# Kernel optimization log

Hardware: AMD Instinct MI355X
Metric: run time of the kernel (lower is better)

## Reference

```python
import jax, jax.numpy as jnp
import numpy as np

B, T, C, H = 4, 2048, 1024, 16
HD = C // H  # head_dim = 64


def setup_inputs() -> dict:
    key = jax.random.key(0)
    ks = jax.random.split(key, 6)
    s_in = 1.0 / np.sqrt(C)
    x = jax.random.normal(ks[0], (B, T, C), dtype=jnp.float32)
    # per-head projection weights, stacked over heads: [H, C, HD]
    Wq = jax.random.uniform(ks[1], (H, C, HD), dtype=jnp.float32, minval=-s_in, maxval=s_in)
    Wk = jax.random.uniform(ks[2], (H, C, HD), dtype=jnp.float32, minval=-s_in, maxval=s_in)
    Wv = jax.random.uniform(ks[3], (H, C, HD), dtype=jnp.float32, minval=-s_in, maxval=s_in)
    # output projection (torch Linear: weight [out,in], bias [out])
    Wp = jax.random.uniform(ks[4], (C, C), dtype=jnp.float32, minval=-s_in, maxval=s_in)
    bp = jax.random.uniform(ks[5], (C,), dtype=jnp.float32, minval=-s_in, maxval=s_in)
    return {"x": x, "Wq": Wq, "Wk": Wk, "Wv": Wv, "Wp": Wp, "bp": bp}


def reference(x, Wq, Wk, Wv, Wp, bp):
    Bx, Tx, Cx = x.shape
    scale = Cx ** 0.5  # NOTE: original scales by embed_dim**0.5, not head_dim**0.5
    q = jnp.einsum('btc,hcd->bhtd', x, Wq)
    k = jnp.einsum('btc,hcd->bhtd', x, Wk)
    v = jnp.einsum('btc,hcd->bhtd', x, Wv)
    # original: einsum('btc,bTc->bTt', q, k) -> logits[b, i, j] = q[b, j] . k[b, i]
    logits = jnp.einsum('bhjd,bhid->bhij', q, k) / scale
    causal = jnp.tril(jnp.ones((Tx, Tx), dtype=bool))  # mask j > i
    logits = jnp.where(causal[None, None], logits, jnp.float32(-jnp.inf))
    weights = jax.nn.softmax(logits, axis=-1)  # [B,H,T,T], the returned attention maps
    # original: einsum('btt,btc->btc', weights, value) -> diagonal of weights scales value
    diag = jnp.diagonal(weights, axis1=-2, axis2=-1)  # [B,H,T]
    attn = diag[..., None] * v  # [B,H,T,HD]
    cat = attn.transpose(0, 2, 1, 3).reshape(Bx, Tx, Cx)  # concat heads on last dim
    out = cat @ Wp.T + bp  # dropout p=0.0 -> identity
    return out, weights
```

## Files before the change

kernel.cpp:

```cpp
#include <hip/hip_runtime.h>


#define NB 4
#define NT 2048
#define NC 1024
#define NH 16
#define NHD 64
#define BH (NB * NH)
typedef unsigned short ushort_t;
#define SLAB ((size_t)NT * (size_t)NT)

typedef __attribute__((ext_vector_type(8))) short short8;
typedef __attribute__((ext_vector_type(4))) float f32x4;

__device__ __forceinline__ ushort_t f2bf(float f) {
    unsigned int x = __float_as_uint(f);
    x += 0x7fffu + ((x >> 16) & 1u);
    return (ushort_t)(x >> 16);
}
__device__ __forceinline__ float bf2f(ushort_t u) {
    return __uint_as_float(((unsigned int)u) << 16);
}

#define GLD_LDS16(g, l) \
    __builtin_amdgcn_global_load_lds( \
        (const __attribute__((address_space(1))) unsigned int*)(g), \
        (__attribute__((address_space(3))) unsigned int*)(l), 16, 0, 0)

__global__ __launch_bounds__(256) void cvt_x(
    const float* __restrict__ x, ushort_t* __restrict__ xbf)
{
    const size_t o = ((size_t)blockIdx.x * 256 + threadIdx.x) * 4;
    float4 u = *(const float4*)(x + o);
    ushort4 v;
    v.x = f2bf(u.x); v.y = f2bf(u.y); v.z = f2bf(u.z); v.w = f2bf(u.w);
    *(ushort4*)(xbf + o) = v;
}

__global__ __launch_bounds__(256) void cvt_w(
    const float* __restrict__ Wq, const float* __restrict__ Wk,
    const float* __restrict__ Wv, ushort_t* __restrict__ Wt)
{
    const int o = blockIdx.x * 256 + threadIdx.x;
    const int sel = o >> 20;
    const int h = (o >> 16) & 15;
    const int idx = o & 65535;
    const int d = idx >> 10, c = idx & 1023;
    const float* W = (sel == 0 ? Wq : (sel == 1 ? Wk : Wv));
    Wt[o] = f2bf(W[(size_t)h * 65536 + (size_t)c * 64 + d]);
}

__global__ __launch_bounds__(256) void cvt_wp(
    const float* __restrict__ Wp, ushort_t* __restrict__ Wpb)
{
    const size_t o = ((size_t)blockIdx.x * 256 + threadIdx.x) * 4;
    float4 u = *(const float4*)(Wp + o);
    ushort4 v;
    v.x = f2bf(u.x); v.y = f2bf(u.y); v.z = f2bf(u.z); v.w = f2bf(u.w);
    *(ushort4*)(Wpb + o) = v;
}

__global__ __launch_bounds__(256) void qkv_gemm2(
    const ushort_t* __restrict__ xbf, const ushort_t* __restrict__ Wt,
    ushort_t* __restrict__ qo, ushort_t* __restrict__ ko, ushort_t* __restrict__ vo)
{
    __shared__ ushort_t smA[128 * 64];
    __shared__ ushort_t smB[128 * 64];
    const int n0 = blockIdx.x * 128;
    const int m0 = blockIdx.y * 128;
    const int tid = threadIdx.x;
    const int wid = tid >> 6, l = tid & 63, lr = l & 15, lg = l >> 4;
    const int wr = wid >> 1, wc = wid & 1;

    const int srow = wid * 32 + (l >> 3);
    const int scol0 = ((l & 7) ^ (srow & 7)) * 8;

    f32x4 acc[4][4];
    #pragma unroll
    for (int i = 0; i < 4; ++i)
        #pragma unroll
        for (int j = 0; j < 4; ++j) acc[i][j] = (f32x4){0.f, 0.f, 0.f, 0.f};

    for (int k0 = 0; k0 < NC; k0 += 64) {
        #pragma unroll
        for (int j = 0; j < 4; ++j) {
            const int row = srow + j * 8;
            GLD_LDS16(xbf + (size_t)(m0 + row) * NC + k0 + scol0,
                      &smA[wid * 2048 + j * 512]);
            GLD_LDS16(Wt + (size_t)(n0 + row) * NC + k0 + scol0,
                      &smB[wid * 2048 + j * 512]);
        }
        __syncthreads();
        short8 a[4][2], b[4][2];
        #pragma unroll
        for (int mi = 0; mi < 4; ++mi) {
            const int rowA = 64 * wr + 16 * mi + lr;
            const int sw = (rowA & 7) * 8;
            a[mi][0] = *(const short8*)&smA[rowA * 64 + ((8 * lg) ^ sw)];
            a[mi][1] = *(const short8*)&smA[rowA * 64 + ((32 + 8 * lg) ^ sw)];
        }
        #pragma unroll
        for (int ni = 0; ni < 4; ++ni) {
            const int rowB = 64 * wc + 16 * ni + lr;
            const int sw = (rowB & 7) * 8;
            b[ni][0] = *(const short8*)&smB[rowB * 64 + ((8 * lg) ^ sw)];
            b[ni][1] = *(const short8*)&smB[rowB * 64 + ((32 + 8 * lg) ^ sw)];
        }
        #pragma unroll
        for (int mi = 0; mi < 4; ++mi)
            #pragma unroll
            for (int ni = 0; ni < 4; ++ni) {
                acc[mi][ni] = __builtin_amdgcn_mfma_f32_16x16x32_bf16(
                    a[mi][0], b[ni][0], acc[mi][ni], 0, 0, 0);
                acc[mi][ni] = __builtin_amdgcn_mfma_f32_16x16x32_bf16(
                    a[mi][1], b[ni][1], acc[mi][ni], 0, 0, 0);
            }
        __syncthreads();
    }
    const int selh = blockIdx.x * 2 + wc;
    const int sel = selh >> 4, h = selh & 15;
    ushort_t* outp = (sel == 0 ? qo : (sel == 1 ? ko : vo));
    #pragma unroll
    for (int mi = 0; mi < 4; ++mi) {
        #pragma unroll
        for (int r = 0; r < 4; ++r) {
            const int m = m0 + 64 * wr + 16 * mi + 4 * lg + r;
            const int bb = m >> 11, tt = m & 2047;
            ushort_t* orow = outp + ((size_t)(bb * NH + h) * NT + tt) * NHD;
            #pragma unroll
            for (int ni = 0; ni < 4; ++ni)
                orow[16 * ni + lr] = f2bf(acc[mi][ni][r]);
        }
    }
}

__global__ __launch_bounds__(256) void scores_mfma(
    const ushort_t* __restrict__ q, const ushort_t* __restrict__ k,
    float* __restrict__ w, float* __restrict__ diag)
{
    __shared__ ushort_t smQ[64 * 64];
    const int ib = blockIdx.x, bh = blockIdx.y;
    const int tid = threadIdx.x;
    const int wid = tid >> 6, l = tid & 63, lr = l & 15, lg = l >> 4;
    const int i0 = ib * 64;
    const ushort_t* kb = k + (size_t)bh * (NT * NHD);
    const ushort_t* qb = q + (size_t)bh * (NT * NHD);
    float* wbase = w + (size_t)bh * SLAB;

    short8 af0, af1;
    {
        const ushort_t* kp = kb + (size_t)(i0 + wid * 16 + lr) * NHD + 8 * lg;
        af0 = *(const short8*)kp;
        af1 = *(const short8*)(kp + 32);
    }
    const int gi_base = i0 + wid * 16 + 4 * lg;

    const int srlo = l >> 3;
    const int scol = ((l & 7) ^ srlo) * 8;

    float lsum[4] = {0.f, 0.f, 0.f, 0.f};
    for (int jt = 0; jt <= ib; ++jt) {
        #pragma unroll
        for (int j = 0; j < 2; ++j) {
            const int row = wid * 16 + j * 8 + srlo;
            GLD_LDS16(qb + (size_t)(jt * 64 + row) * NHD + scol,
                      &smQ[(wid * 16 + j * 8) * 64]);
        }
        __syncthreads();
        #pragma unroll
        for (int nt = 0; nt < 4; ++nt) {
            const int rowB = nt * 16 + lr;
            const int sw = (rowB & 7) * 8;
            const short8 b0 = *(const short8*)&smQ[rowB * 64 + ((8 * lg) ^ sw)];
            const short8 b1 = *(const short8*)&smQ[rowB * 64 + ((32 + 8 * lg) ^ sw)];
            f32x4 acc = {0,0,0,0};
            acc = __builtin_amdgcn_mfma_f32_16x16x32_bf16(af0, b0, acc, 0, 0, 0);
            acc = __builtin_amdgcn_mfma_f32_16x16x32_bf16(af1, b1, acc, 0, 0, 0);
            const int gj = jt * 64 + nt * 16 + lr;
            #pragma unroll
            for (int r = 0; r < 4; ++r) {
                float e = __expf(acc[r] * 0.03125f);
                lsum[r] += (gj <= gi_base + r) ? e : 0.f;
            }
        }
        __syncthreads();
    }
    float linv[4];
    #pragma unroll
    for (int r = 0; r < 4; ++r) {
        float v = lsum[r];
        v += __shfl_xor(v, 1);
        v += __shfl_xor(v, 2);
        v += __shfl_xor(v, 4);
        v += __shfl_xor(v, 8);
        linv[r] = 1.0f / v;
    }
    for (int jt = 0; jt <= ib; ++jt) {
        #pragma unroll
        for (int j = 0; j < 2; ++j) {
            const int row = wid * 16 + j * 8 + srlo;
            GLD_LDS16(qb + (size_t)(jt * 64 + row) * NHD + scol,
                      &smQ[(wid * 16 + j * 8) * 64]);
        }
        __syncthreads();
        #pragma unroll
        for (int nt = 0; nt < 4; ++nt) {
            const int rowB = nt * 16 + lr;
            const int sw = (rowB & 7) * 8;
            const short8 b0 = *(const short8*)&smQ[rowB * 64 + ((8 * lg) ^ sw)];
            const short8 b1 = *(const short8*)&smQ[rowB * 64 + ((32 + 8 * lg) ^ sw)];
            f32x4 acc = {0,0,0,0};
            acc = __builtin_amdgcn_mfma_f32_16x16x32_bf16(af0, b0, acc, 0, 0, 0);
            acc = __builtin_amdgcn_mfma_f32_16x16x32_bf16(af1, b1, acc, 0, 0, 0);
            const int gj = jt * 64 + nt * 16 + lr;
            #pragma unroll
            for (int r = 0; r < 4; ++r) {
                const int gi = gi_base + r;
                float e = __expf(acc[r] * 0.03125f) * linv[r];
                e = (gj <= gi) ? e : 0.f;
                wbase[(size_t)gi * NT + gj] = e;
                if (gj == gi) diag[(size_t)bh * NT + gi] = e;
            }
        }
        __syncthreads();
    }
    for (int jt = ib + 1; jt < NT / 64; ++jt) {
        #pragma unroll
        for (int it = 0; it < 4; ++it) {
            const int row = i0 + wid * 16 + it * 4 + lg;
            *(float4*)&wbase[(size_t)row * NT + jt * 64 + lr * 4] =
                make_float4(0.f, 0.f, 0.f, 0.f);
        }
    }
}

__global__ __launch_bounds__(256) void scale_v(
    const ushort_t* __restrict__ v, const float* __restrict__ diag,
    ushort_t* __restrict__ vd)
{
    const size_t o8 = (size_t)blockIdx.x * 256 + threadIdx.x;
    const size_t o = o8 * 8;
    const size_t bht = o >> 6;
    const float dg = diag[bht];
    short8 u = *(const short8*)(v + o);
    short8 r;
    #pragma unroll
    for (int j = 0; j < 8; ++j)
        r[j] = (short)f2bf(bf2f((ushort_t)u[j]) * dg);
    *(short8*)(vd + o) = r;
}

__global__ __launch_bounds__(256) void out_gemm(
    const ushort_t* __restrict__ vd, const ushort_t* __restrict__ Wpb,
    const float* __restrict__ bpv, float* __restrict__ out)
{
    __shared__ ushort_t smA[128 * 64];
    __shared__ ushort_t smB[128 * 64];
    const int n0 = blockIdx.x * 128;
    const int m0 = blockIdx.y * 128;
    const int tid = threadIdx.x;
    const int wid = tid >> 6, l = tid & 63, lr = l & 15, lg = l >> 4;
    const int wr = wid >> 1, wc = wid & 1;

    const int srow = wid * 32 + (l >> 3);
    const int scol0 = ((l & 7) ^ (srow & 7)) * 8;

    f32x4 acc[4][4];
    #pragma unroll
    for (int i = 0; i < 4; ++i)
        #pragma unroll
        for (int j = 0; j < 4; ++j) acc[i][j] = (f32x4){0.f, 0.f, 0.f, 0.f};

    for (int k0 = 0; k0 < NC; k0 += 64) {
        const int h = k0 >> 6;
        #pragma unroll
        for (int j = 0; j < 4; ++j) {
            const int row = srow + j * 8;
            const int m = m0 + row, bb = m >> 11, tt = m & 2047;
            GLD_LDS16(vd + ((size_t)(bb * NH + h) * NT + tt) * NHD + scol0,
                      &smA[wid * 2048 + j * 512]);
            GLD_LDS16(Wpb + (size_t)(n0 + row) * NC + k0 + scol0,
                      &smB[wid * 2048 + j * 512]);
        }
        __syncthreads();
        short8 a[4][2], b[4][2];
        #pragma unroll
        for (int mi = 0; mi < 4; ++mi) {
            const int rowA = 64 * wr + 16 * mi + lr;
            const int sw = (rowA & 7) * 8;
            a[mi][0] = *(const short8*)&smA[rowA * 64 + ((8 * lg) ^ sw)];
            a[mi][1] = *(const short8*)&smA[rowA * 64 + ((32 + 8 * lg) ^ sw)];
        }
        #pragma unroll
        for (int ni = 0; ni < 4; ++ni) {
            const int rowB = 64 * wc + 16 * ni + lr;
            const int sw = (rowB & 7) * 8;
            b[ni][0] = *(const short8*)&smB[rowB * 64 + ((8 * lg) ^ sw)];
            b[ni][1] = *(const short8*)&smB[rowB * 64 + ((32 + 8 * lg) ^ sw)];
        }
        #pragma unroll
        for (int mi = 0; mi < 4; ++mi)
            #pragma unroll
            for (int ni = 0; ni < 4; ++ni) {
                acc[mi][ni] = __builtin_amdgcn_mfma_f32_16x16x32_bf16(
                    a[mi][0], b[ni][0], acc[mi][ni], 0, 0, 0);
                acc[mi][ni] = __builtin_amdgcn_mfma_f32_16x16x32_bf16(
                    a[mi][1], b[ni][1], acc[mi][ni], 0, 0, 0);
            }
        __syncthreads();
    }
    float bias[4];
    #pragma unroll
    for (int ni = 0; ni < 4; ++ni) bias[ni] = bpv[n0 + 64 * wc + 16 * ni + lr];
    #pragma unroll
    for (int mi = 0; mi < 4; ++mi) {
        #pragma unroll
        for (int r = 0; r < 4; ++r) {
            const int m = m0 + 64 * wr + 16 * mi + 4 * lg + r;
            float* orow = out + (size_t)m * NC + n0 + 64 * wc;
            #pragma unroll
            for (int ni = 0; ni < 4; ++ni)
                orow[16 * ni + lr] = acc[mi][ni][r] + bias[ni];
        }
    }
}

extern "C" void kernel_launch(void* const* d_in, const int* in_sizes, int n_in,
                              void* d_out, int out_size, void* d_ws, size_t ws_size,
                              hipStream_t stream)
{
    const float* x  = (const float*)d_in[0];
    const float* Wq = (const float*)d_in[1];
    const float* Wk = (const float*)d_in[2];
    const float* Wv = (const float*)d_in[3];
    const float* Wp = (const float*)d_in[4];
    const float* bp = (const float*)d_in[5];

    float* out = (float*)d_out;
    float* w = out + (size_t)NB * NT * NC;

    ushort_t* xbf = (ushort_t*)d_ws;
    ushort_t* Wt  = xbf + (size_t)NB * NT * NC;
    ushort_t* qs  = Wt + (size_t)3 * NH * NHD * NC;
    ushort_t* ks  = qs + (size_t)BH * NT * NHD;
    ushort_t* vs  = ks + (size_t)BH * NT * NHD;
    float* diag   = (float*)(vs + (size_t)BH * NT * NHD);
    ushort_t* Wpb = (ushort_t*)(diag + (size_t)BH * NT);
    ushort_t* vd  = Wpb + (size_t)NC * NC;

    cvt_x<<<(NB * NT * NC) / 1024, 256, 0, stream>>>(x, xbf);
    cvt_w<<<(3 * NH * NHD * NC) / 256, 256, 0, stream>>>(Wq, Wk, Wv, Wt);
    cvt_wp<<<(NC * NC) / 1024, 256, 0, stream>>>(Wp, Wpb);
    qkv_gemm2<<<dim3(24, 64), 256, 0, stream>>>(xbf, Wt, qs, ks, vs);
    scores_mfma<<<dim3(NT / 64, BH), 256, 0, stream>>>(qs, ks, w, diag);
    scale_v<<<(BH * NT * NHD) / (256 * 8), 256, 0, stream>>>(vs, diag, vd);
    out_gemm<<<dim3(8, 64), 256, 0, stream>>>(vd, Wpb, bp, out);
}
```

Measured before the change: 451.3 us.

## Fuse diag scaling into output GEMM, double-buffer Q tiles, use nontemporal stores

Removes the separate scale_v kernel by applying the softmax diagonal scale to V while staging it into shared memory in the output GEMM. The scores kernel now double-buffers Q tiles in LDS, prefetching the next tile during compute. The attention-weight, zero-fill and output writes become nontemporal stores to reduce cache pollution on the large streaming write. In exchange, the V loads in the GEMM go through registers instead of direct-to-LDS loads, and the kernel uses more LDS.

```diff
diff --git a/kernel.cpp b/kernel.cpp
--- a/kernel.cpp
+++ b/kernel.cpp
@@ -138,7 +138,7 @@
     const ushort_t* __restrict__ q, const ushort_t* __restrict__ k,
     float* __restrict__ w, float* __restrict__ diag)
 {
-    __shared__ ushort_t smQ[64 * 64];
+    __shared__ ushort_t smQ[2][64 * 64];
     const int ib = blockIdx.x, bh = blockIdx.y;
     const int tid = threadIdx.x;
     const int wid = tid >> 6, l = tid & 63, lr = l & 15, lg = l >> 4;
@@ -158,21 +158,26 @@
     const int srlo = l >> 3;
     const int scol = ((l & 7) ^ srlo) * 8;
 
+    #define STAGEQ(buf, jt)                                                  \
+        _Pragma("unroll")                                                    \
+        for (int j = 0; j < 2; ++j) {                                        \
+            const int row_ = wid * 16 + j * 8 + srlo;                        \
+            GLD_LDS16(qb + (size_t)((jt) * 64 + row_) * NHD + scol,          \
+                      &smQ[buf][(wid * 16 + j * 8) * 64]);                   \
+        }
+
     float lsum[4] = {0.f, 0.f, 0.f, 0.f};
+    STAGEQ(0, 0);
+    __syncthreads();
     for (int jt = 0; jt <= ib; ++jt) {
-        #pragma unroll
-        for (int j = 0; j < 2; ++j) {
-            const int row = wid * 16 + j * 8 + srlo;
-            GLD_LDS16(qb + (size_t)(jt * 64 + row) * NHD + scol,
-                      &smQ[(wid * 16 + j * 8) * 64]);
-        }
-        __syncthreads();
+        const int cur = jt & 1;
+        if (jt < ib) { STAGEQ(cur ^ 1, jt + 1); }
         #pragma unroll
         for (int nt = 0; nt < 4; ++nt) {
             const int rowB = nt * 16 + lr;
             const int sw = (rowB & 7) * 8;
-            const short8 b0 = *(const short8*)&smQ[rowB * 64 + ((8 * lg) ^ sw)];
-            const short8 b1 = *(const short8*)&smQ[rowB * 64 + ((32 + 8 * lg) ^ sw)];
+            const short8 b0 = *(const short8*)&smQ[cur][rowB * 64 + ((8 * lg) ^ sw)];
+            const short8 b1 = *(const short8*)&smQ[cur][rowB * 64 + ((32 + 8 * lg) ^ sw)];
             f32x4 acc = {0,0,0,0};
             acc = __builtin_amdgcn_mfma_f32_16x16x32_bf16(af0, b0, acc, 0, 0, 0);
             acc = __builtin_amdgcn_mfma_f32_16x16x32_bf16(af1, b1, acc, 0, 0, 0);
@@ -195,20 +200,17 @@
         v += __shfl_xor(v, 8);
         linv[r] = 1.0f / v;
     }
+    STAGEQ(0, 0);
+    __syncthreads();
     for (int jt = 0; jt <= ib; ++jt) {
-        #pragma unroll
-        for (int j = 0; j < 2; ++j) {
-            const int row = wid * 16 + j * 8 + srlo;
-            GLD_LDS16(qb + (size_t)(jt * 64 + row) * NHD + scol,
-                      &smQ[(wid * 16 + j * 8) * 64]);
-        }
-        __syncthreads();
+        const int cur = jt & 1;
+        if (jt < ib) { STAGEQ(cur ^ 1, jt + 1); }
         #pragma unroll
         for (int nt = 0; nt < 4; ++nt) {
             const int rowB = nt * 16 + lr;
             const int sw = (rowB & 7) * 8;
-            const short8 b0 = *(const short8*)&smQ[rowB * 64 + ((8 * lg) ^ sw)];
-            const short8 b1 = *(const short8*)&smQ[rowB * 64 + ((32 + 8 * lg) ^ sw)];
+            const short8 b0 = *(const short8*)&smQ[cur][rowB * 64 + ((8 * lg) ^ sw)];
+            const short8 b1 = *(const short8*)&smQ[cur][rowB * 64 + ((32 + 8 * lg) ^ sw)];
             f32x4 acc = {0,0,0,0};
             acc = __builtin_amdgcn_mfma_f32_16x16x32_bf16(af0, b0, acc, 0, 0, 0);
             acc = __builtin_amdgcn_mfma_f32_16x16x32_bf16(af1, b1, acc, 0, 0, 0);
@@ -218,41 +220,28 @@
                 const int gi = gi_base + r;
                 float e = __expf(acc[r] * 0.03125f) * linv[r];
                 e = (gj <= gi) ? e : 0.f;
-                wbase[(size_t)gi * NT + gj] = e;
+                __builtin_nontemporal_store(e, &wbase[(size_t)gi * NT + gj]);
                 if (gj == gi) diag[(size_t)bh * NT + gi] = e;
             }
         }
         __syncthreads();
     }
+    #undef STAGEQ
+    const f32x4 z4 = {0.f, 0.f, 0.f, 0.f};
     for (int jt = ib + 1; jt < NT / 64; ++jt) {
         #pragma unroll
         for (int it = 0; it < 4; ++it) {
             const int row = i0 + wid * 16 + it * 4 + lg;
-            *(float4*)&wbase[(size_t)row * NT + jt * 64 + lr * 4] =
-                make_float4(0.f, 0.f, 0.f, 0.f);
-        }
-    }
-}
-
-__global__ __launch_bounds__(256) void scale_v(
-    const ushort_t* __restrict__ v, const float* __restrict__ diag,
-    ushort_t* __restrict__ vd)
-{
-    const size_t o8 = (size_t)blockIdx.x * 256 + threadIdx.x;
-    const size_t o = o8 * 8;
-    const size_t bht = o >> 6;
-    const float dg = diag[bht];
-    short8 u = *(const short8*)(v + o);
-    short8 r;
-    #pragma unroll
-    for (int j = 0; j < 8; ++j)
-        r[j] = (short)f2bf(bf2f((ushort_t)u[j]) * dg);
-    *(short8*)(vd + o) = r;
+            f32x4* p = (f32x4*)&wbase[(size_t)row * NT + jt * 64 + lr * 4];
+            __builtin_nontemporal_store(z4, p);
+        }
+    }
 }
 
 __global__ __launch_bounds__(256) void out_gemm(
-    const ushort_t* __restrict__ vd, const ushort_t* __restrict__ Wpb,
-    const float* __restrict__ bpv, float* __restrict__ out)
+    const ushort_t* __restrict__ vs, const float* __restrict__ diag,
+    const ushort_t* __restrict__ Wpb, const float* __restrict__ bpv,
+    float* __restrict__ out)
 {
     __shared__ ushort_t smA[128 * 64];
     __shared__ ushort_t smB[128 * 64];
@@ -275,12 +264,21 @@
         const int h = k0 >> 6;
         #pragma unroll
         for (int j = 0; j < 4; ++j) {
+            GLD_LDS16(Wpb + (size_t)(n0 + srow + j * 8) * NC + k0 + scol0,
+                      &smB[wid * 2048 + j * 512]);
+        }
+        #pragma unroll
+        for (int j = 0; j < 4; ++j) {
             const int row = srow + j * 8;
             const int m = m0 + row, bb = m >> 11, tt = m & 2047;
-            GLD_LDS16(vd + ((size_t)(bb * NH + h) * NT + tt) * NHD + scol0,
-                      &smA[wid * 2048 + j * 512]);
-            GLD_LDS16(Wpb + (size_t)(n0 + row) * NC + k0 + scol0,
-                      &smB[wid * 2048 + j * 512]);
+            const size_t bhT = (size_t)(bb * NH + h) * NT + tt;
+            const short8 u = *(const short8*)(vs + bhT * NHD + (l & 7) * 8);
+            const float dg = diag[bhT];
+            short8 sc;
+            #pragma unroll
+            for (int e = 0; e < 8; ++e)
+                sc[e] = (short)f2bf(bf2f((ushort_t)u[e]) * dg);
+            *(short8*)&smA[row * 64 + scol0] = sc;
         }
         __syncthreads();
         short8 a[4][2], b[4][2];
@@ -320,7 +318,8 @@
             float* orow = out + (size_t)m * NC + n0 + 64 * wc;
             #pragma unroll
             for (int ni = 0; ni < 4; ++ni)
-                orow[16 * ni + lr] = acc[mi][ni][r] + bias[ni];
+                __builtin_nontemporal_store(acc[mi][ni][r] + bias[ni],
+                                            &orow[16 * ni + lr]);
         }
     }
 }
@@ -346,13 +345,11 @@
     ushort_t* vs  = ks + (size_t)BH * NT * NHD;
     float* diag   = (float*)(vs + (size_t)BH * NT * NHD);
     ushort_t* Wpb = (ushort_t*)(diag + (size_t)BH * NT);
-    ushort_t* vd  = Wpb + (size_t)NC * NC;
 
     cvt_x<<<(NB * NT * NC) / 1024, 256, 0, stream>>>(x, xbf);
     cvt_w<<<(3 * NH * NHD * NC) / 256, 256, 0, stream>>>(Wq, Wk, Wv, Wt);
     cvt_wp<<<(NC * NC) / 1024, 256, 0, stream>>>(Wp, Wpb);
     qkv_gemm2<<<dim3(24, 64), 256, 0, stream>>>(xbf, Wt, qs, ks, vs);
     scores_mfma<<<dim3(NT / 64, BH), 256, 0, stream>>>(qs, ks, w, diag);
-    scale_v<<<(BH * NT * NHD) / (256 * 8), 256, 0, stream>>>(vs, diag, vd);
-    out_gemm<<<dim3(8, 64), 256, 0, stream>>>(vd, Wpb, bp, out);
-}
+    out_gemm<<<dim3(8, 64), 256, 0, stream>>>(vs, diag, Wpb, bp, out);
+}
```

Result: no change. 454.3 us (+0.7%).
